# Optimization experiments

Hardware: AMD Instinct MI355X
Metric: run time of the kernel (lower is better)

The kernel has to match this reference:

```python
import jax, jax.numpy as jnp
import numpy as np

N, D, H, O, E, K = 16384, 512, 512, 64, 8, 2


def _layernorm(x, g, b, eps=1e-5):
    mu = jnp.mean(x, axis=-1, keepdims=True)
    var = jnp.var(x, axis=-1, keepdims=True)
    return (x - mu) * jax.lax.rsqrt(var + eps) * g + b


def _gelu(x):
    return jax.nn.gelu(x, approximate=False)  # torch nn.GELU default (erf)


def setup_inputs() -> dict:
    key = jax.random.key(0)
    ks = jax.random.split(key, 20)
    s = 0.02
    return {
        "x": jax.random.normal(ks[0], (N, D), jnp.float32),
        # gate: Linear(D,H) -> LN(H) -> GELU -> Linear(H,E)
        "g_w1": jax.random.normal(ks[1], (D, H), jnp.float32) * s,
        "g_b1": jnp.zeros((H,), jnp.float32),
        "g_ln_g": jnp.ones((H,), jnp.float32),
        "g_ln_b": jnp.zeros((H,), jnp.float32),
        "g_w2": jax.random.normal(ks[2], (H, E), jnp.float32) * s,
        "g_b2": jnp.zeros((E,), jnp.float32),
        # experts (stacked over E): Linear(D,H)+LN+GELU, Linear(H,H)+LN+GELU, Linear(H,O)
        "e_w1": jax.random.normal(ks[3], (E, D, H), jnp.float32) * s,
        "e_b1": jnp.zeros((E, H), jnp.float32),
        "e_ln1_g": jnp.ones((E, H), jnp.float32),
        "e_ln1_b": jnp.zeros((E, H), jnp.float32),
        "e_w2": jax.random.normal(ks[4], (E, H, H), jnp.float32) * s,
        "e_b2": jnp.zeros((E, H), jnp.float32),
        "e_ln2_g": jnp.ones((E, H), jnp.float32),
        "e_ln2_b": jnp.zeros((E, H), jnp.float32),
        "e_w3": jax.random.normal(ks[5], (E, H, O), jnp.float32) * s,
        "e_b3": jnp.zeros((E, O), jnp.float32),
        # output projection Linear(O,O)
        "p_w": jax.random.normal(ks[6], (O, O), jnp.float32) * s,
        "p_b": jnp.zeros((O,), jnp.float32),
    }


def reference(x, g_w1, g_b1, g_ln_g, g_ln_b, g_w2, g_b2,
              e_w1, e_b1, e_ln1_g, e_ln1_b, e_w2, e_b2, e_ln2_g, e_ln2_b,
              e_w3, e_b3, p_w, p_b):
    n = x.shape[0]
    # --- gate ---
    gh = _gelu(_layernorm(x @ g_w1 + g_b1, g_ln_g, g_ln_b))
    gate_logits = gh @ g_w2 + g_b2                      # [N, E]
    gate_weights = jax.nn.softmax(gate_logits, axis=-1)
    top_k_weights, top_k_indices = jax.lax.top_k(gate_weights, K)
    top_k_weights = top_k_weights / jnp.sum(top_k_weights, axis=-1, keepdims=True)
    # dense per-token expert weights [N, E] (sum of top-k weights routed to each expert)
    w_dense = jnp.zeros((n, e_w1.shape[0]), x.dtype).at[
        jnp.arange(n)[:, None], top_k_indices].add(top_k_weights)
    # --- all experts on all tokens (faithful to dense loop) ---
    h1 = _gelu(_layernorm(jnp.einsum('nd,edh->enh', x, e_w1) + e_b1[:, None, :],
                          e_ln1_g[:, None, :], e_ln1_b[:, None, :]))
    h2 = _gelu(_layernorm(jnp.einsum('enh,ehk->enk', h1, e_w2) + e_b2[:, None, :],
                          e_ln2_g[:, None, :], e_ln2_b[:, None, :]))
    expert_out = jnp.einsum('enh,eho->eno', h2, e_w3) + e_b3[:, None, :]  # [E, N, O]
    combined = jnp.einsum('ne,eno->no', w_dense, expert_out)              # [N, O]
    output = combined @ p_w + p_b
    expert_usage = jnp.mean(gate_weights, axis=0)
    return (output, gate_weights, top_k_indices, top_k_weights, expert_usage)
```

## Files before the change

### kernel.cpp

```cpp
#include <hip/hip_runtime.h>
#include <hip/hip_bf16.h>

#define N_TOK 16384
#define MAX_SLOTS 34080
#define MAX_BLOCKS 216

typedef __attribute__((ext_vector_type(8))) short bf16x8;
typedef __attribute__((ext_vector_type(4))) float f32x4;
typedef unsigned short u16;
typedef unsigned char u8;
typedef long i64;

#define V_WAIT(N) asm volatile("s_waitcnt vmcnt(" #N ")" ::: "memory")
#define LGKM0()   asm volatile("s_waitcnt lgkmcnt(0)" ::: "memory")

__device__ __forceinline__ u16 f2bf(float f) {
  __hip_bfloat16 h = __float2bfloat16(f);
  union { __hip_bfloat16 b; u16 u; } c; c.b = h; return c.u;
}
__device__ __forceinline__ float bfbits2f(u16 u) {
  return __uint_as_float(((unsigned)u) << 16);
}
__device__ __forceinline__ float gelu_erf(float x) {
  return 0.5f * x * (1.0f + erff(x * 0.70710678118654752f));
}
__device__ __forceinline__ float gelu_fast(float x) {
  float u = x * (0.79788456f + 0.035677408f * x * x);
  float ex;
  asm("v_exp_f32 %0, %1" : "=v"(ex) : "v"(-2.8853901f * u));
  float den = 1.0f + ex;
  float r;
  asm("v_rcp_f32 %0, %1" : "=v"(r) : "v"(den));
  return x * r;
}
__device__ __forceinline__ u8 f2fp8(float f) {
  return (u8)(__builtin_amdgcn_cvt_pk_fp8_f32(f, f, 0, false) & 0xff);
}
__device__ __forceinline__ void gload16(const void* g, char* lds) {
  __builtin_amdgcn_global_load_lds(
      (const __attribute__((address_space(1))) void*)g,
      (__attribute__((address_space(3))) void*)lds, 16, 0, 0);
}

__global__ __launch_bounds__(256) void prep_x(const float* __restrict__ x,
                                              u16* __restrict__ xbf,
                                              u16* __restrict__ xlo,
                                              u8* __restrict__ xf8) {
  size_t i = (size_t)blockIdx.x * 256 + threadIdx.x;
  float4 v = ((const float4*)x)[i];
  float a[4] = {v.x, v.y, v.z, v.w};
  union { u16 us[4]; unsigned long long ll; } hb, lb;
#pragma unroll
  for (int j = 0; j < 4; ++j) {
    u16 hu = f2bf(a[j]);
    hb.us[j] = hu;
    lb.us[j] = f2bf(a[j] - bfbits2f(hu));
  }
  *(unsigned long long*)(xbf + i * 4) = hb.ll;
  *(unsigned long long*)(xlo + i * 4) = lb.ll;
  int w8 = __builtin_amdgcn_cvt_pk_fp8_f32(a[0], a[1], 0, false);
  w8 = __builtin_amdgcn_cvt_pk_fp8_f32(a[2], a[3], w8, true);
  *(int*)(xf8 + i * 4) = w8;
}

template <int C>
__global__ __launch_bounds__(256) void pack_w_f8(const float* __restrict__ src,
                                                 u8* __restrict__ dst, int R) {
  __shared__ float tl[64][65];
  const int e = blockIdx.z;
  const int k0 = blockIdx.x * 64, n0 = blockIdx.y * 64;
  const float* s = src + (size_t)e * R * C;
  const int tr = threadIdx.x >> 2;
  const int tc4 = (threadIdx.x & 3) * 16;
#pragma unroll
  for (int j = 0; j < 4; ++j) {
    float4 v = *(const float4*)(s + (size_t)(k0 + tr) * C + n0 + tc4 + j * 4);
    tl[tr][tc4 + j * 4 + 0] = v.x;
    tl[tr][tc4 + j * 4 + 1] = v.y;
    tl[tr][tc4 + j * 4 + 2] = v.z;
    tl[tr][tc4 + j * 4 + 3] = v.w;
  }
  __syncthreads();
  const int nl = threadIdx.x >> 2;
  const int kl = (threadIdx.x & 3) * 16;
  const int n = n0 + nl;
  const int T = R / 64;
  const int t = (k0 + kl) >> 6;
  const int q = ((k0 + kl) >> 4) & 3;
  const int p = q ^ ((n >> 1) & 3);
  uint4 o;
  unsigned w[4];
#pragma unroll
  for (int j = 0; j < 4; ++j) {
    int ww = __builtin_amdgcn_cvt_pk_fp8_f32(tl[kl + 4 * j][nl],
                                             tl[kl + 4 * j + 1][nl], 0, false);
    ww = __builtin_amdgcn_cvt_pk_fp8_f32(tl[kl + 4 * j + 2][nl],
                                         tl[kl + 4 * j + 3][nl], ww, true);
    w[j] = (unsigned)ww;
  }
  o.x = w[0]; o.y = w[1]; o.z = w[2]; o.w = w[3];
  *(uint4*)(dst + (((size_t)e * T + t) * C + n) * 64 + p * 16) = o;
}

__global__ __launch_bounds__(256) void prep_wcat(const float* __restrict__ gw1,
                                                 u16* __restrict__ wp) {
  int idx = blockIdx.x * 256 + threadIdx.x;
  int p = idx & 3;
  int n = (idx >> 2) & 511;
  int t = idx >> 11;
  int q = p ^ ((n >> 1) & 3);
  int k0 = t * 32 + q * 8;
  union { u16 us[8]; unsigned long long ll[2]; } o;
#pragma unroll
  for (int j = 0; j < 8; ++j) {
    int k = k0 + j;
    u16 v;
    if (k < 512) {
      v = f2bf(gw1[k * 512 + n]);
    } else if (k < 1024) {
      float w = gw1[(k - 512) * 512 + n];
      v = f2bf(w - bfbits2f(f2bf(w)));
    } else {
      v = f2bf(gw1[(k - 1024) * 512 + n]);
    }
    o.us[j] = v;
  }
  unsigned long long* d = (unsigned long long*)(wp + (size_t)idx * 8);
  d[0] = o.ll[0];
  d[1] = o.ll[1];
}

__global__ __launch_bounds__(256) void prep_w2t(const float* __restrict__ gw2,
                                                float* __restrict__ w2t) {
  int i = blockIdx.x * 256 + threadIdx.x;
  int e = i >> 9, k = i & 511;
  w2t[i] = gw2[k * 8 + e];
}

template <int FM>
__global__ __launch_bounds__(512, 2) void gemm_gate(
    const u16* __restrict__ A, const u16* __restrict__ A2,
    const u16* __restrict__ Wp, int klen, long osplit,
    float* __restrict__ outf) {
  constexpr int BM = FM * 32;
  constexpr int AG = FM * 2;
  constexpr int ABYTES = BM * 64;
  constexpr int BUF = ABYTES + 32768;
  constexpr int NL = AG + 32;
  constexpr int L = (NL + 7) / 8;
  constexpr int TSU = 16384;
  extern __shared__ char smem[];

  const int tid = threadIdx.x;
  const int lane = tid & 63;
  const int wv = tid >> 6;
  const int wm = (wv & 1) * (FM * 16);
  const int wn = (wv >> 1) * 128;
  const int l15 = lane & 15;
  const int lk = lane >> 4;
  const int swzk16 = (lk ^ ((l15 >> 1) & 3)) << 4;

  const int row0 = blockIdx.x * BM;
  const int kbase = blockIdx.y * klen;
  const int kt0 = kbase >> 5;

  const int lrq = lane >> 2;
  const int cse = (((lane & 3) ^ ((lane >> 3) & 3)) << 3);
  size_t off[L];
  int ldsoff[L], typ[L];
#pragma unroll
  for (int i = 0; i < L; ++i) {
    int id = wv + 8 * i;
    if (id >= NL) { typ[i] = 2; off[i] = 0; ldsoff[i] = 0; continue; }
    if (id < AG) {
      off[i] = (size_t)(row0 + id * 16 + lrq) * 512 + cse;
      ldsoff[i] = id * 1024 + lane * 16;
      typ[i] = 0;
    } else {
      int bg = id - AG;
      off[i] = (size_t)bg * 512 + lane * 8;
      ldsoff[i] = ABYTES + bg * 1024 + lane * 16;
      typ[i] = 1;
    }
  }

  auto STAGE = [&](int t, char* b) {
    const int kg = kbase + t * 32;
    const u16* Aseg = A;
    int kc = kg;
    if (kg >= 1024) { Aseg = A2; kc = kg - 1024; }
    else if (kg >= 512) kc = kg - 512;
    const u16* Bt = Wp + (size_t)(kt0 + t) * TSU;
#pragma unroll
    for (int i = 0; i < L; ++i) {
      if (typ[i] == 0)      gload16(Aseg + off[i] + kc, b + ldsoff[i]);
      else if (typ[i] == 1) gload16(Bt + off[i], b + ldsoff[i]);
    }
  };

  f32x4 acc[FM][8];
#pragma unroll
  for (int i = 0; i < FM; ++i)
#pragma unroll
    for (int j = 0; j < 8; ++j) acc[i][j] = (f32x4){0.f, 0.f, 0.f, 0.f};

  const int nt = klen / 32;
  V_WAIT(0);
  STAGE(0, smem);
  STAGE(1, smem + BUF);
  STAGE(2, smem + 2 * BUF);

  int bsel = 0;
  for (int t = 0; t < nt; ++t) {
    if (t < nt - 2)       V_WAIT(10);
    else if (t == nt - 2) V_WAIT(5);
    else                  V_WAIT(0);
    __builtin_amdgcn_s_barrier();
    char* cur = smem + bsel * BUF;
    char* cB = cur + ABYTES;
    bf16x8 af[FM];
#pragma unroll
    for (int fm = 0; fm < FM; ++fm)
      af[fm] = *(const bf16x8*)(cur + (wm + fm * 16 + l15) * 64 + swzk16);
#pragma unroll
    for (int fn = 0; fn < 8; ++fn) {
      bf16x8 bv = *(const bf16x8*)(cB + (wn + fn * 16 + l15) * 64 + swzk16);
#pragma unroll
      for (int fm = 0; fm < FM; ++fm)
        acc[fm][fn] = __builtin_amdgcn_mfma_f32_16x16x32_bf16(
            af[fm], bv, acc[fm][fn], 0, 0, 0);
    }
    LGKM0();
    __builtin_amdgcn_s_barrier();
    if (t + 3 < nt) STAGE(t + 3, cur);
    bsel = (bsel == 2) ? 0 : bsel + 1;
  }

  float* dst = outf + (size_t)blockIdx.y * osplit;
#pragma unroll
  for (int fm = 0; fm < FM; ++fm)
#pragma unroll
    for (int r = 0; r < 4; ++r) {
      size_t rowg = (size_t)(row0 + wm + fm * 16 + lk * 4 + r);
#pragma unroll
      for (int fn = 0; fn < 8; ++fn)
        dst[rowg * 512 + wn + fn * 16 + l15] = acc[fm][fn][r];
    }
}

template <int GATHER>
__global__ __launch_bounds__(512, 2) void gemm_f8(
    const u8* __restrict__ A, const u8* __restrict__ Wp, long w_estride,
    const float* __restrict__ bias, const float* __restrict__ lng,
    const float* __restrict__ lnb, u8* __restrict__ outb,
    const int* __restrict__ slot_token, const int* __restrict__ blk_e,
    const int* __restrict__ blk_tok0) {
  constexpr int FM = 5, BM = 160, AG = 10;
  constexpr int ABYTES = BM * 64;
  constexpr int BUF = ABYTES + 32768;
  constexpr int NL = AG + 32;
  constexpr int L = 6;
  extern __shared__ char smem[];

  const int tid = threadIdx.x;
  const int lane = tid & 63;
  const int wv = tid >> 6;
  const int wm = (wv & 1) * 80;
  const int wn = (wv >> 1) * 128;
  const int l15 = lane & 15;
  const int lk = lane >> 4;
  const int sx = (l15 >> 1) & 3;
  const int swz0 = (((lk >> 1) ^ sx) << 4) + (lk & 1) * 8;
  const int swz1 = ((((lk >> 1) + 2) ^ sx) << 4) + (lk & 1) * 8;

  int e = blk_e[blockIdx.x];
  if (e < 0) return;
  const int row0 = blk_tok0[blockIdx.x];
  const u8* We = Wp + (size_t)e * w_estride;

  const int lrq = lane >> 2;
  const int csb = (((lane & 3) ^ ((lane >> 3) & 3)) << 4);
  size_t off[L];
  int ldsoff[L], typ[L];
#pragma unroll
  for (int i = 0; i < L; ++i) {
    int id = wv + 8 * i;
    if (id >= NL) { typ[i] = 2; off[i] = 0; ldsoff[i] = 0; continue; }
    if (id < AG) {
      int lr = id * 16 + lrq;
      long grow = GATHER ? (long)slot_token[row0 + lr] : (long)(row0 + lr);
      off[i] = (size_t)grow * 512 + csb;
      ldsoff[i] = id * 1024 + lane * 16;
      typ[i] = 0;
    } else {
      int bg = id - AG;
      off[i] = (size_t)bg * 1024 + lane * 16;
      ldsoff[i] = ABYTES + bg * 1024 + lane * 16;
      typ[i] = 1;
    }
  }

  float bias_v[8], g_v[8], b_v[8];
  const float* be = bias + (size_t)e * 512;
  const float* ge = lng + (size_t)e * 512;
  const float* bbe = lnb + (size_t)e * 512;
#pragma unroll
  for (int fn = 0; fn < 8; ++fn) {
    int col = wn + fn * 16 + l15;
    bias_v[fn] = be[col]; g_v[fn] = ge[col]; b_v[fn] = bbe[col];
  }

  auto STAGE = [&](int t, char* b) {
    const u8* Bt = We + (size_t)t * 32768;
#pragma unroll
    for (int i = 0; i < L; ++i) {
      if (typ[i] == 0)      gload16(A + off[i] + t * 64, b + ldsoff[i]);
      else if (typ[i] == 1) gload16(Bt + off[i], b + ldsoff[i]);
    }
  };

  f32x4 acc[FM][8];
#pragma unroll
  for (int i = 0; i < FM; ++i)
#pragma unroll
    for (int j = 0; j < 8; ++j) acc[i][j] = (f32x4){0.f, 0.f, 0.f, 0.f};

  constexpr int nt = 8;
  V_WAIT(0);
  STAGE(0, smem);
  STAGE(1, smem + BUF);
  STAGE(2, smem + 2 * BUF);

  int bsel = 0;
  for (int t = 0; t < nt; ++t) {
    if (t < nt - 2)       { if (wv < 2) V_WAIT(12); else V_WAIT(10); }
    else if (t == nt - 2) { if (wv < 2) V_WAIT(6);  else V_WAIT(5); }
    else                  V_WAIT(0);
    __builtin_amdgcn_s_barrier();
    char* cur = smem + bsel * BUF;
    char* cB = cur + ABYTES;
#pragma unroll
    for (int s = 0; s < 2; ++s) {
      const int sw = s ? swz1 : swz0;
      i64 af[FM];
#pragma unroll
      for (int fm = 0; fm < FM; ++fm)
        af[fm] = *(const i64*)(cur + (wm + fm * 16 + l15) * 64 + sw);
#pragma unroll
      for (int fn = 0; fn < 8; ++fn) {
        i64 bv = *(const i64*)(cB + (wn + fn * 16 + l15) * 64 + sw);
#pragma unroll
        for (int fm = 0; fm < FM; ++fm)
          acc[fm][fn] = __builtin_amdgcn_mfma_f32_16x16x32_fp8_fp8(
              af[fm], bv, acc[fm][fn], 0, 0, 0);
      }
    }
    LGKM0();
    __builtin_amdgcn_s_barrier();
    if (t + 3 < nt) STAGE(t + 3, cur);
    bsel = (bsel == 2) ? 0 : bsel + 1;
  }

#pragma unroll
  for (int fm = 0; fm < FM; ++fm)
#pragma unroll
    for (int fn = 0; fn < 8; ++fn)
#pragma unroll
      for (int r = 0; r < 4; ++r) acc[fm][fn][r] += bias_v[fn];

  float* redS1 = (float*)smem;
  float* redS2 = redS1 + 4 * BM;
  const int g = wv >> 1;
#pragma unroll
  for (int fm = 0; fm < FM; ++fm)
#pragma unroll
    for (int r = 0; r < 4; ++r) {
      float a1 = 0.f, a2 = 0.f;
#pragma unroll
      for (int fn = 0; fn < 8; ++fn) {
        float v = acc[fm][fn][r];
        a1 += v; a2 += v * v;
      }
#pragma unroll
      for (int m = 1; m < 16; m <<= 1) {
        a1 += __shfl_xor(a1, m, 64);
        a2 += __shfl_xor(a2, m, 64);
      }
      if (l15 == 0) {
        int row = wm + fm * 16 + lk * 4 + r;
        redS1[g * BM + row] = a1;
        redS2[g * BM + row] = a2;
      }
    }
  __syncthreads();
#pragma unroll
  for (int fm = 0; fm < FM; ++fm)
#pragma unroll
    for (int r = 0; r < 4; ++r) {
      int row = wm + fm * 16 + lk * 4 + r;
      float S1 = 0.f, S2 = 0.f;
#pragma unroll
      for (int q = 0; q < 4; ++q) {
        S1 += redS1[q * BM + row];
        S2 += redS2[q * BM + row];
      }
      float mu = S1 * (1.0f / 512.0f);
      float var = S2 * (1.0f / 512.0f) - mu * mu;
      float rs = rsqrtf(var + 1e-5f);
      size_t rowg = (size_t)(row0 + row);
#pragma unroll
      for (int fn = 0; fn < 8; ++fn) {
        int col = wn + fn * 16 + l15;
        float v = (acc[fm][fn][r] - mu) * rs * g_v[fn] + b_v[fn];
        outb[rowg * 512 + col] = f2fp8(gelu_fast(v));
      }
    }
}

__global__ __launch_bounds__(256) void gate2_topk(
    const float* __restrict__ gh0, const float* __restrict__ gh1,
    const float* __restrict__ b1, const float* __restrict__ lng,
    const float* __restrict__ lnb, const float* __restrict__ w2t,
    const float* __restrict__ b2, float* __restrict__ gwout,
    float* __restrict__ idxout, float* __restrict__ tkwout) {
  const int lane = threadIdx.x & 63;
  const int wv = threadIdx.x >> 6;
  const int t = blockIdx.x * 4 + wv;
  const int c0 = lane * 8;
  float v[8];
  {
    float4 a0 = *(const float4*)(gh0 + (size_t)t * 512 + c0);
    float4 a1 = *(const float4*)(gh0 + (size_t)t * 512 + c0 + 4);
    float4 h0 = *(const float4*)(gh1 + (size_t)t * 512 + c0);
    float4 h1 = *(const float4*)(gh1 + (size_t)t * 512 + c0 + 4);
    float4 bb0 = *(const float4*)(b1 + c0);
    float4 bb1 = *(const float4*)(b1 + c0 + 4);
    v[0] = a0.x + h0.x + bb0.x; v[1] = a0.y + h0.y + bb0.y;
    v[2] = a0.z + h0.z + bb0.z; v[3] = a0.w + h0.w + bb0.w;
    v[4] = a1.x + h1.x + bb1.x; v[5] = a1.y + h1.y + bb1.y;
    v[6] = a1.z + h1.z + bb1.z; v[7] = a1.w + h1.w + bb1.w;
  }
  float s1 = 0.f, s2 = 0.f;
#pragma unroll
  for (int j = 0; j < 8; ++j) { s1 += v[j]; s2 += v[j] * v[j]; }
#pragma unroll
  for (int m = 1; m < 64; m <<= 1) {
    s1 += __shfl_xor(s1, m, 64);
    s2 += __shfl_xor(s2, m, 64);
  }
  float mu = s1 * (1.0f / 512.0f);
  float var = s2 * (1.0f / 512.0f) - mu * mu;
  float rs = rsqrtf(var + 1e-5f);
  float y[8];
  {
    float4 g0 = *(const float4*)(lng + c0);
    float4 g1 = *(const float4*)(lng + c0 + 4);
    float4 q0 = *(const float4*)(lnb + c0);
    float4 q1 = *(const float4*)(lnb + c0 + 4);
    float gg[8] = {g0.x, g0.y, g0.z, g0.w, g1.x, g1.y, g1.z, g1.w};
    float qq[8] = {q0.x, q0.y, q0.z, q0.w, q1.x, q1.y, q1.z, q1.w};
#pragma unroll
    for (int j = 0; j < 8; ++j)
      y[j] = gelu_erf((v[j] - mu) * rs * gg[j] + qq[j]);
  }
  float logit[8];
#pragma unroll
  for (int e = 0; e < 8; ++e) {
    const float4* wr = (const float4*)(w2t + e * 512 + c0);
    float4 w0 = wr[0], w1 = wr[1];
    float p = y[0] * w0.x + y[1] * w0.y + y[2] * w0.z + y[3] * w0.w +
              y[4] * w1.x + y[5] * w1.y + y[6] * w1.z + y[7] * w1.w;
#pragma unroll
    for (int m = 1; m < 64; m <<= 1) p += __shfl_xor(p, m, 64);
    logit[e] = p + b2[e];
  }
  if (lane == 0) {
    float mx = logit[0];
#pragma unroll
    for (int e = 1; e < 8; ++e) mx = fmaxf(mx, logit[e]);
    float w[8], ssum = 0.f;
#pragma unroll
    for (int e = 0; e < 8; ++e) { w[e] = expf(logit[e] - mx); ssum += w[e]; }
    float inv = 1.0f / ssum;
#pragma unroll
    for (int e = 0; e < 8; ++e) w[e] *= inv;
    float w1v = -1.f, w2v = -1.f; int i1 = 0, i2 = 0;
#pragma unroll
    for (int e = 0; e < 8; ++e) {
      float vv = w[e];
      if (vv > w1v)      { w2v = w1v; i2 = i1; w1v = vv; i1 = e; }
      else if (vv > w2v) { w2v = vv; i2 = e; }
    }
    float s = w1v + w2v;
#pragma unroll
    for (int e = 0; e < 8; ++e) gwout[t * 8 + e] = w[e];
    idxout[t * 2] = (float)i1; idxout[t * 2 + 1] = (float)i2;
    tkwout[t * 2] = w1v / s;   tkwout[t * 2 + 1] = w2v / s;
  }
}

__global__ __launch_bounds__(256) void usage_k(const float* __restrict__ gw,
                                               float* __restrict__ usage) {
  __shared__ float r[256];
  int e = blockIdx.x;
  float s = 0.f;
  for (int t = threadIdx.x; t < N_TOK; t += 256) s += gw[t * 8 + e];
  r[threadIdx.x] = s;
  __syncthreads();
  for (int st = 128; st > 0; st >>= 1) {
    if (threadIdx.x < st) r[threadIdx.x] += r[threadIdx.x + st];
    __syncthreads();
  }
  if (threadIdx.x == 0) usage[e] = r[0] * (1.0f / (float)N_TOK);
}

__global__ __launch_bounds__(256) void count_hist(const float* __restrict__ idxout,
                                                  int* __restrict__ blk_cnt) {
  __shared__ int h[8];
  if (threadIdx.x < 8) h[threadIdx.x] = 0;
  __syncthreads();
  int t = blockIdx.x * 256 + threadIdx.x;
  int e0 = (int)idxout[t * 2], e1 = (int)idxout[t * 2 + 1];
  atomicAdd(&h[e0], 1);
  atomicAdd(&h[e1], 1);
  __syncthreads();
  if (threadIdx.x < 8) blk_cnt[blockIdx.x * 8 + threadIdx.x] = h[threadIdx.x];
}

__global__ __launch_bounds__(512) void k_offsets2(
    const int* __restrict__ blk_cnt, int* __restrict__ sbase,
    int* __restrict__ blk_e, int* __restrict__ blk_tok0) {
  __shared__ int cnt[64][8];
  __shared__ int ecnt[8];
  __shared__ int offs[8];
  const int tid = threadIdx.x;
  cnt[tid >> 3][tid & 7] = blk_cnt[tid];
  __syncthreads();
  if (tid < 8) {
    int s = 0;
    for (int b = 0; b < 64; ++b) s += cnt[b][tid];
    ecnt[tid] = s;
  }
  __syncthreads();
  if (tid == 0) {
    int off = 0;
    for (int e = 0; e < 8; ++e) {
      offs[e] = off;
      off += ((ecnt[e] + 159) / 160) * 160;
    }
  }
  __syncthreads();
  {
    int b = tid >> 3, e = tid & 7;
    int s = offs[e];
    for (int bp = 0; bp < b; ++bp) s += cnt[bp][e];
    sbase[tid] = s;
  }
  for (int b = tid; b < MAX_BLOCKS; b += 512) {
    int acc = 0, be = -1, bt = 0;
#pragma unroll
    for (int e = 0; e < 8; ++e) {
      int nbe = (ecnt[e] + 159) / 160;
      if (b >= acc && b < acc + nbe) { be = e; bt = offs[e] + (b - acc) * 160; }
      acc += nbe;
    }
    blk_e[b] = be;
    blk_tok0[b] = bt;
  }
}

__global__ __launch_bounds__(256) void k_padinit(int* __restrict__ slot_token,
                                                 float* __restrict__ slot_w) {
  int i = blockIdx.x * 256 + threadIdx.x;
  if (i < MAX_SLOTS) { slot_token[i] = 0; slot_w[i] = 0.f; }
}

__global__ __launch_bounds__(256) void k_scatter2(
    const float* __restrict__ idxout, const float* __restrict__ tkwout,
    const int* __restrict__ sbase, int* __restrict__ slot_token,
    float* __restrict__ slot_w, int* __restrict__ tok_slot) {
  __shared__ int lpos[8];
  if (threadIdx.x < 8) lpos[threadIdx.x] = 0;
  __syncthreads();
  int t = blockIdx.x * 256 + threadIdx.x;
#pragma unroll
  for (int k = 0; k < 2; ++k) {
    int e = (int)idxout[t * 2 + k];
    int lr = atomicAdd(&lpos[e], 1);
    int s = sbase[blockIdx.x * 8 + e] + lr;
    slot_token[s] = t;
    slot_w[s] = tkwout[t * 2 + k];
    tok_slot[t * 2 + k] = s;
  }
}

__global__ __launch_bounds__(512) void gemm3_f8(
    const u8* __restrict__ h, const u8* __restrict__ w3p,
    const float* __restrict__ b3, const float* __restrict__ slot_w,
    const int* __restrict__ blk_e, const int* __restrict__ blk_tok0,
    float* __restrict__ eo) {
  constexpr int ABYTES = 10240;
  constexpr int BUF = ABYTES + 4096;
  __shared__ char smem[3 * BUF];
  int e = blk_e[blockIdx.x];
  if (e < 0) return;
  const int row0 = blk_tok0[blockIdx.x];

  const int tid = threadIdx.x;
  const int lane = tid & 63;
  const int wv = tid >> 6;
  const int wm = (wv & 1) * 80;
  const int wn = (wv >> 1) * 16;
  const int l15 = lane & 15, lk = lane >> 4;
  const int sx = (l15 >> 1) & 3;
  const int swz0 = (((lk >> 1) ^ sx) << 4) + (lk & 1) * 8;
  const int swz1 = ((((lk >> 1) + 2) ^ sx) << 4) + (lk & 1) * 8;
  const u8* we = w3p + (size_t)e * 32768;

  const int lrq = lane >> 2;
  const int csb = (((lane & 3) ^ ((lane >> 3) & 3)) << 4);
  size_t off[2];
  int ldsoff[2], typ[2];
#pragma unroll
  for (int i = 0; i < 2; ++i) {
    int id = wv + 8 * i;
    if (id >= 14) { typ[i] = 2; off[i] = 0; ldsoff[i] = 0; continue; }
    if (id < 10) {
      off[i] = (size_t)(row0 + id * 16 + lrq) * 512 + csb;
      ldsoff[i] = id * 1024 + lane * 16;
      typ[i] = 0;
    } else {
      int bg = id - 10;
      off[i] = (size_t)bg * 1024 + lane * 16;
      ldsoff[i] = ABYTES + bg * 1024 + lane * 16;
      typ[i] = 1;
    }
  }

  float b3v = b3[e * 64 + wn + l15];
  float swr[5][4];
#pragma unroll
  for (int fm = 0; fm < 5; ++fm)
#pragma unroll
    for (int r = 0; r < 4; ++r)
      swr[fm][r] = slot_w[row0 + wm + fm * 16 + lk * 4 + r];

  auto STAGE = [&](int t, char* b) {
#pragma unroll
    for (int i = 0; i < 2; ++i) {
      if (typ[i] == 0)      gload16(h + off[i] + t * 64, b + ldsoff[i]);
      else if (typ[i] == 1) gload16(we + (size_t)t * 4096 + off[i], b + ldsoff[i]);
    }
  };

  f32x4 acc[5];
#pragma unroll
  for (int j = 0; j < 5; ++j) acc[j] = (f32x4){0.f, 0.f, 0.f, 0.f};

  V_WAIT(0);
  STAGE(0, smem);
  STAGE(1, smem + BUF);
  STAGE(2, smem + 2 * BUF);

  int bsel = 0;
  for (int t = 0; t < 8; ++t) {
    if (t < 6)       { if (wv < 6) V_WAIT(4); else V_WAIT(2); }
    else if (t == 6) { if (wv < 6) V_WAIT(2); else V_WAIT(1); }
    else             V_WAIT(0);
    __builtin_amdgcn_s_barrier();
    char* cur = smem + bsel * BUF;
    char* cB = cur + ABYTES;
#pragma unroll
    for (int s = 0; s < 2; ++s) {
      const int sw = s ? swz1 : swz0;
      i64 bv = *(const i64*)(cB + (wn + l15) * 64 + sw);
#pragma unroll
      for (int fm = 0; fm < 5; ++fm) {
        i64 a = *(const i64*)(cur + (wm + fm * 16 + l15) * 64 + sw);
        acc[fm] = __builtin_amdgcn_mfma_f32_16x16x32_fp8_fp8(a, bv, acc[fm],
                                                             0, 0, 0);
      }
    }
    LGKM0();
    __builtin_amdgcn_s_barrier();
    if (t + 3 < 8) STAGE(t + 3, cur);
    bsel = (bsel == 2) ? 0 : bsel + 1;
  }

#pragma unroll
  for (int fm = 0; fm < 5; ++fm)
#pragma unroll
    for (int r = 0; r < 4; ++r) {
      int row = wm + fm * 16 + lk * 4 + r;
      eo[(size_t)(row0 + row) * 64 + wn + l15] = swr[fm][r] * (acc[fm][r] + b3v);
    }
}

__global__ __launch_bounds__(256) void combine_proj(
    const float* __restrict__ eo, const int* __restrict__ tok_slot,
    const float* __restrict__ pw, const float* __restrict__ pb,
    float* __restrict__ outp) {
  __shared__ float cs[64][68];
  __shared__ float pws[64][68];
  const int t0 = blockIdx.x * 64;
  const int tq = threadIdx.x & 3;
  const int tt = threadIdx.x >> 2;
#pragma unroll
  for (int j = 0; j < 4; ++j) {
    float4 v = *(const float4*)(pw + tt * 64 + tq * 16 + j * 4);
    *(float4*)&pws[tt][tq * 16 + j * 4] = v;
  }
  {
    int t = t0 + tt;
    int s1 = tok_slot[t * 2], s2 = tok_slot[t * 2 + 1];
#pragma unroll
    for (int j = 0; j < 4; ++j) {
      float4 a = *(const float4*)(eo + (size_t)s1 * 64 + tq * 16 + j * 4);
      float4 b = *(const float4*)(eo + (size_t)s2 * 64 + tq * 16 + j * 4);
      float4 c = {a.x + b.x, a.y + b.y, a.z + b.z, a.w + b.w};
      *(float4*)&cs[tt][tq * 16 + j * 4] = c;
    }
  }
  __syncthreads();
  float o[16];
#pragma unroll
  for (int i = 0; i < 16; ++i) o[i] = 0.f;
  for (int j = 0; j < 64; ++j) {
    float c = cs[tt][j];
#pragma unroll
    for (int q4 = 0; q4 < 4; ++q4) {
      float4 p = *(const float4*)&pws[j][tq * 16 + q4 * 4];
      o[q4 * 4 + 0] += c * p.x;
      o[q4 * 4 + 1] += c * p.y;
      o[q4 * 4 + 2] += c * p.z;
      o[q4 * 4 + 3] += c * p.w;
    }
  }
#pragma unroll
  for (int i = 0; i < 16; ++i)
    outp[(size_t)(t0 + tt) * 64 + tq * 16 + i] = o[i] + pb[tq * 16 + i];
}

extern "C" void kernel_launch(void* const* d_in, const int* in_sizes, int n_in,
                              void* d_out, int out_size, void* d_ws, size_t ws_size,
                              hipStream_t stream) {
  const float* x      = (const float*)d_in[0];
  const float* g_w1   = (const float*)d_in[1];
  const float* g_b1   = (const float*)d_in[2];
  const float* g_lng  = (const float*)d_in[3];
  const float* g_lnb  = (const float*)d_in[4];
  const float* g_w2   = (const float*)d_in[5];
  const float* g_b2   = (const float*)d_in[6];
  const float* e_w1   = (const float*)d_in[7];
  const float* e_b1   = (const float*)d_in[8];
  const float* e_ln1g = (const float*)d_in[9];
  const float* e_ln1b = (const float*)d_in[10];
  const float* e_w2   = (const float*)d_in[11];
  const float* e_b2   = (const float*)d_in[12];
  const float* e_ln2g = (const float*)d_in[13];
  const float* e_ln2b = (const float*)d_in[14];
  const float* e_w3   = (const float*)d_in[15];
  const float* e_b3   = (const float*)d_in[16];
  const float* p_w    = (const float*)d_in[17];
  const float* p_b    = (const float*)d_in[18];

  char* ws = (char*)d_ws;
  u16*   x_bf  = (u16*)(ws);
  u16*   x_lo  = (u16*)(ws + (16ull << 20));
  u8*    x_f8  = (u8*)(ws + (32ull << 20));
  u8*    e_w1p = (u8*)(ws + (40ull << 20));
  u8*    e_w2p = (u8*)(ws + (42ull << 20));
  u8*    e_w3p = (u8*)(ws + (44ull << 20));
  u16*   wcat  = (u16*)(ws + (45ull << 20));
  float* w2t   = (float*)(ws + (47ull << 20));
  float* gh0   = (float*)(ws + (48ull << 20));
  float* gh1   = (float*)(ws + (80ull << 20));
  u8*    h     = (u8*)(ws + (48ull << 20));
  float* eo    = (float*)(ws + (112ull << 20));
  int*   slot_token = (int*)(ws + (121ull << 20));
  float* slot_w     = (float*)(ws + (121ull << 20) + (1ull << 18));
  int*   tok_slot   = (int*)(ws + (121ull << 20) + (2ull << 18));
  int*   blk_cnt    = (int*)(ws + (122ull << 20));
  int*   sbase      = blk_cnt + 512;
  int*   blk_e      = blk_cnt + 1024;
  int*   blk_tok0   = blk_cnt + 2048;
  if (ws_size < (123ull << 20)) return;

  float* fout = (float*)d_out;
  float* o_output = fout;
  float* o_gatew  = fout + 1048576;
  float* o_idx    = fout + 1179648;
  float* o_topw   = fout + 1212416;
  float* o_usage  = fout + 1245184;

  (void)hipFuncSetAttribute((const void*)gemm_gate<4>,
                            hipFuncAttributeMaxDynamicSharedMemorySize, 122880);
  (void)hipFuncSetAttribute((const void*)gemm_f8<1>,
                            hipFuncAttributeMaxDynamicSharedMemorySize, 129024);
  (void)hipFuncSetAttribute((const void*)gemm_f8<0>,
                            hipFuncAttributeMaxDynamicSharedMemorySize, 129024);

  prep_x<<<8192, 256, 0, stream>>>(x, x_bf, x_lo, x_f8);
  pack_w_f8<512><<<dim3(8, 8, 8), 256, 0, stream>>>(e_w1, e_w1p, 512);
  pack_w_f8<512><<<dim3(8, 8, 8), 256, 0, stream>>>(e_w2, e_w2p, 512);
  pack_w_f8<64><<<dim3(8, 1, 8), 256, 0, stream>>>(e_w3, e_w3p, 512);
  prep_wcat<<<384, 256, 0, stream>>>(g_w1, wcat);
  prep_w2t<<<16, 256, 0, stream>>>(g_w2, w2t);

  gemm_gate<4><<<dim3(N_TOK / 128, 2), 512, 122880, stream>>>(
      x_bf, x_lo, wcat, 768, (long)N_TOK * 512, gh0);
  gate2_topk<<<N_TOK / 4, 256, 0, stream>>>(gh0, gh1, g_b1, g_lng, g_lnb,
                                            w2t, g_b2, o_gatew, o_idx, o_topw);
  usage_k<<<8, 256, 0, stream>>>(o_gatew, o_usage);

  count_hist<<<64, 256, 0, stream>>>(o_idx, blk_cnt);
  k_offsets2<<<1, 512, 0, stream>>>(blk_cnt, sbase, blk_e, blk_tok0);
  k_padinit<<<(MAX_SLOTS + 255) / 256, 256, 0, stream>>>(slot_token, slot_w);
  k_scatter2<<<64, 256, 0, stream>>>(o_idx, o_topw, sbase, slot_token, slot_w,
                                     tok_slot);

  gemm_f8<1><<<MAX_BLOCKS, 512, 129024, stream>>>(
      x_f8, e_w1p, 262144, e_b1, e_ln1g, e_ln1b, h,
      slot_token, blk_e, blk_tok0);
  gemm_f8<0><<<MAX_BLOCKS, 512, 129024, stream>>>(
      h, e_w2p, 262144, e_b2, e_ln2g, e_ln2b, h,
      slot_token, blk_e, blk_tok0);
  gemm3_f8<<<MAX_BLOCKS, 512, 0, stream>>>(h, e_w3p, e_b3, slot_w, blk_e,
                                           blk_tok0, eo);
  combine_proj<<<N_TOK / 64, 256, 0, stream>>>(eo, tok_slot, p_w, p_b, o_output);
}
```

Baseline: 235.1 us.

## Permute fp8 K layout so MFMA operands load as 16-byte LDS reads

Reorders the K dimension within each 64-wide chunk of the fp8 activations and weights (the kperm mapping in the x prep, weight packing and layer-1 output stores) so that the two K=32 MFMA steps for a lane sit in one contiguous 16-byte segment. The GEMM inner loops then issue one 128-bit LDS read per fragment instead of two 64-bit reads with separate swizzles. This halves the LDS instruction count in the fp8 GEMMs. The cost is scattered byte stores in the epilogue and a producer/consumer layout contract that must match exactly across kernels.

New measurement: 225.6 us. -4.0%, faster.

```diff
diff --git a/kernel.cpp b/kernel.cpp
--- a/kernel.cpp
+++ b/kernel.cpp
@@ -7,6 +7,7 @@
 
 typedef __attribute__((ext_vector_type(8))) short bf16x8;
 typedef __attribute__((ext_vector_type(4))) float f32x4;
+typedef __attribute__((ext_vector_type(2))) long i64x2;
 typedef unsigned short u16;
 typedef unsigned char u8;
 typedef long i64;
@@ -36,6 +37,10 @@
 __device__ __forceinline__ u8 f2fp8(float f) {
   return (u8)(__builtin_amdgcn_cvt_pk_fp8_f32(f, f, 0, false) & 0xff);
 }
+__device__ __forceinline__ int kperm(int k64) {
+  return (k64 < 32) ? (((k64 >> 3) << 4) + (k64 & 7))
+                    : ((((k64 - 32) >> 3) << 4) + 8 + (k64 & 7));
+}
 __device__ __forceinline__ void gload16(const void* g, char* lds) {
   __builtin_amdgcn_global_load_lds(
       (const __attribute__((address_space(1))) void*)g,
@@ -60,7 +65,10 @@
   *(unsigned long long*)(xlo + i * 4) = lb.ll;
   int w8 = __builtin_amdgcn_cvt_pk_fp8_f32(a[0], a[1], 0, false);
   w8 = __builtin_amdgcn_cvt_pk_fp8_f32(a[2], a[3], w8, true);
-  *(int*)(xf8 + i * 4) = w8;
+  size_t f = i * 4;
+  int k = (int)(f & 511);
+  size_t base = (f & ~(size_t)511) + (k & ~63);
+  *(int*)(xf8 + base + kperm(k & 63)) = w8;
 }
 
 template <int C>
@@ -82,23 +90,26 @@
   }
   __syncthreads();
   const int nl = threadIdx.x >> 2;
-  const int kl = (threadIdx.x & 3) * 16;
+  const int q = threadIdx.x & 3;
   const int n = n0 + nl;
+  const int p = q ^ ((n >> 1) & 3);
   const int T = R / 64;
-  const int t = (k0 + kl) >> 6;
-  const int q = ((k0 + kl) >> 4) & 3;
-  const int p = q ^ ((n >> 1) & 3);
+  const int t = k0 >> 6;
   uint4 o;
-  unsigned w[4];
-#pragma unroll
-  for (int j = 0; j < 4; ++j) {
-    int ww = __builtin_amdgcn_cvt_pk_fp8_f32(tl[kl + 4 * j][nl],
-                                             tl[kl + 4 * j + 1][nl], 0, false);
-    ww = __builtin_amdgcn_cvt_pk_fp8_f32(tl[kl + 4 * j + 2][nl],
-                                         tl[kl + 4 * j + 3][nl], ww, true);
-    w[j] = (unsigned)ww;
-  }
-  o.x = w[0]; o.y = w[1]; o.z = w[2]; o.w = w[3];
+  {
+    int w = __builtin_amdgcn_cvt_pk_fp8_f32(tl[q * 8 + 0][nl], tl[q * 8 + 1][nl], 0, false);
+    w = __builtin_amdgcn_cvt_pk_fp8_f32(tl[q * 8 + 2][nl], tl[q * 8 + 3][nl], w, true);
+    o.x = (unsigned)w;
+    w = __builtin_amdgcn_cvt_pk_fp8_f32(tl[q * 8 + 4][nl], tl[q * 8 + 5][nl], 0, false);
+    w = __builtin_amdgcn_cvt_pk_fp8_f32(tl[q * 8 + 6][nl], tl[q * 8 + 7][nl], w, true);
+    o.y = (unsigned)w;
+    w = __builtin_amdgcn_cvt_pk_fp8_f32(tl[32 + q * 8 + 0][nl], tl[32 + q * 8 + 1][nl], 0, false);
+    w = __builtin_amdgcn_cvt_pk_fp8_f32(tl[32 + q * 8 + 2][nl], tl[32 + q * 8 + 3][nl], w, true);
+    o.z = (unsigned)w;
+    w = __builtin_amdgcn_cvt_pk_fp8_f32(tl[32 + q * 8 + 4][nl], tl[32 + q * 8 + 5][nl], 0, false);
+    w = __builtin_amdgcn_cvt_pk_fp8_f32(tl[32 + q * 8 + 6][nl], tl[32 + q * 8 + 7][nl], w, true);
+    o.w = (unsigned)w;
+  }
   *(uint4*)(dst + (((size_t)e * T + t) * C + n) * 64 + p * 16) = o;
 }
 
@@ -269,9 +280,7 @@
   const int wn = (wv >> 1) * 128;
   const int l15 = lane & 15;
   const int lk = lane >> 4;
-  const int sx = (l15 >> 1) & 3;
-  const int swz0 = (((lk >> 1) ^ sx) << 4) + (lk & 1) * 8;
-  const int swz1 = ((((lk >> 1) + 2) ^ sx) << 4) + (lk & 1) * 8;
+  const int swzk16 = (lk ^ ((l15 >> 1) & 3)) << 4;
 
   int e = blk_e[blockIdx.x];
   if (e < 0) return;
@@ -339,21 +348,21 @@
     __builtin_amdgcn_s_barrier();
     char* cur = smem + bsel * BUF;
     char* cB = cur + ABYTES;
-#pragma unroll
-    for (int s = 0; s < 2; ++s) {
-      const int sw = s ? swz1 : swz0;
-      i64 af[FM];
+    i64x2 af[FM];
+#pragma unroll
+    for (int fm = 0; fm < FM; ++fm)
+      af[fm] = *(const i64x2*)(cur + (wm + fm * 16 + l15) * 64 + swzk16);
+#pragma unroll
+    for (int fn = 0; fn < 8; ++fn) {
+      i64x2 bv = *(const i64x2*)(cB + (wn + fn * 16 + l15) * 64 + swzk16);
 #pragma unroll
       for (int fm = 0; fm < FM; ++fm)
-        af[fm] = *(const i64*)(cur + (wm + fm * 16 + l15) * 64 + sw);
-#pragma unroll
-      for (int fn = 0; fn < 8; ++fn) {
-        i64 bv = *(const i64*)(cB + (wn + fn * 16 + l15) * 64 + sw);
-#pragma unroll
-        for (int fm = 0; fm < FM; ++fm)
-          acc[fm][fn] = __builtin_amdgcn_mfma_f32_16x16x32_fp8_fp8(
-              af[fm], bv, acc[fm][fn], 0, 0, 0);
-      }
+        acc[fm][fn] = __builtin_amdgcn_mfma_f32_16x16x32_fp8_fp8(
+            af[fm].x, bv.x, acc[fm][fn], 0, 0, 0);
+#pragma unroll
+      for (int fm = 0; fm < FM; ++fm)
+        acc[fm][fn] = __builtin_amdgcn_mfma_f32_16x16x32_fp8_fp8(
+            af[fm].y, bv.y, acc[fm][fn], 0, 0, 0);
     }
     LGKM0();
     __builtin_amdgcn_s_barrier();
@@ -412,7 +421,8 @@
       for (int fn = 0; fn < 8; ++fn) {
         int col = wn + fn * 16 + l15;
         float v = (acc[fm][fn][r] - mu) * rs * g_v[fn] + b_v[fn];
-        outb[rowg * 512 + col] = f2fp8(gelu_fast(v));
+        int pos = (col & ~63) + kperm(col & 63);
+        outb[rowg * 512 + pos] = f2fp8(gelu_fast(v));
       }
     }
 }
@@ -612,9 +622,7 @@
   const int wm = (wv & 1) * 80;
   const int wn = (wv >> 1) * 16;
   const int l15 = lane & 15, lk = lane >> 4;
-  const int sx = (l15 >> 1) & 3;
-  const int swz0 = (((lk >> 1) ^ sx) << 4) + (lk & 1) * 8;
-  const int swz1 = ((((lk >> 1) + 2) ^ sx) << 4) + (lk & 1) * 8;
+  const int swzk16 = (lk ^ ((l15 >> 1) & 3)) << 4;
   const u8* we = w3p + (size_t)e * 32768;
 
   const int lrq = lane >> 2;
@@ -670,16 +678,14 @@
     __builtin_amdgcn_s_barrier();
     char* cur = smem + bsel * BUF;
     char* cB = cur + ABYTES;
-#pragma unroll
-    for (int s = 0; s < 2; ++s) {
-      const int sw = s ? swz1 : swz0;
-      i64 bv = *(const i64*)(cB + (wn + l15) * 64 + sw);
-#pragma unroll
-      for (int fm = 0; fm < 5; ++fm) {
-        i64 a = *(const i64*)(cur + (wm + fm * 16 + l15) * 64 + sw);
-        acc[fm] = __builtin_amdgcn_mfma_f32_16x16x32_fp8_fp8(a, bv, acc[fm],
-                                                             0, 0, 0);
-      }
+    i64x2 bv = *(const i64x2*)(cB + (wn + l15) * 64 + swzk16);
+#pragma unroll
+    for (int fm = 0; fm < 5; ++fm) {
+      i64x2 a = *(const i64x2*)(cur + (wm + fm * 16 + l15) * 64 + swzk16);
+      acc[fm] = __builtin_amdgcn_mfma_f32_16x16x32_fp8_fp8(a.x, bv.x, acc[fm],
+                                                           0, 0, 0);
+      acc[fm] = __builtin_amdgcn_mfma_f32_16x16x32_fp8_fp8(a.y, bv.y, acc[fm],
+                                                           0, 0, 0);
     }
     LGKM0();
     __builtin_amdgcn_s_barrier();
```
